# Performance work log

Hardware: AMD Instinct MI355X
Metric: run time of the kernel (lower is better)

The kernel has to match this reference:

```python
import jax, jax.numpy as jnp
import numpy as np
from jax import lax

DOWNSAMPLE = 4.0   # downsample_rate
THRESHOLD = 0.7    # score threshold
NMS_RANGE = 3      # maxpool NMS kernel


def setup_inputs() -> dict:
    key = jax.random.key(0)
    k1, k2 = jax.random.split(key)
    radiace_factor = jax.random.uniform(k1, (8, 80, 192, 192), dtype=jnp.float32)  # class heatmap
    box = jax.random.uniform(k2, (8, 4, 192, 192), dtype=jnp.float32)              # [dx, dy, w, h]
    return {"radiace_factor": radiace_factor, "box": box}


def _nms(heat, kernel):
    # max_pool2d(kernel, stride=1, padding=(kernel-1)//2) == SAME window max
    hmax = lax.reduce_window(heat, -jnp.inf, lax.max,
                             (1, 1, kernel, kernel), (1, 1, 1, 1), 'SAME')
    return heat * (hmax == heat).astype(heat.dtype)


def reference(radiace_factor, box):
    B, C, H, W = radiace_factor.shape
    r = jnp.float32(DOWNSAMPLE)

    heat = _nms(radiace_factor, NMS_RANGE)
    score = heat.max(axis=1)               # [B,H,W] max over categories
    mask = score > THRESHOLD               # [B,H,W] kept peaks

    # grid of (x=col, y=row) matching torch.where(inds)[::-1]
    gx, gy = jnp.meshgrid(jnp.arange(W, dtype=jnp.float32),
                          jnp.arange(H, dtype=jnp.float32), indexing='xy')
    grid = jnp.stack([gx, gy], axis=-1)    # [H,W,2]

    b = jnp.moveaxis(box, 1, -1)           # [B,H,W,4] = (dx,dy,w,h)
    center_xy = (grid + b[..., 0:2]) * r   # [B,H,W,2]
    wh = b[..., 2:4] * r

    lim = jnp.array([W * DOWNSAMPLE, H * DOWNSAMPLE], dtype=jnp.float32)
    x1y1 = jnp.clip(center_xy - wh * 0.5, 0.0, lim)
    x2y2 = jnp.clip(center_xy + wh * 0.5, 0.0, lim)
    boxes = jnp.concatenate([x1y1, x2y2 - x1y1], axis=-1)  # [B,H,W,4] (x1,y1,w,h)

    # Dense, jit-friendly equivalent of the per-batch gather: zero-out non-kept
    m = mask[..., None]
    boxes_kept = jnp.where(m, boxes, 0.0)
    scores_kept = jnp.where(mask, score, 0.0)
    center_kept = jnp.where(m, center_xy, 0.0)
    return boxes_kept, mask, scores_kept, center_kept
```

## Files before the change

kernel.cpp:

```cpp
#include <hip/hip_runtime.h>
#include <math.h>


#define BB 8
#define CC 80
#define HH 192
#define WW 192
#define SS 8
#define NBPIX (BB*HH*WW)

__global__ __launch_bounds__(256) void score_kernel(const float* __restrict__ heat,
                                                    float* __restrict__ part) {
    const int tid  = threadIdx.x;
    const int lane = tid & 63;
    const int wv   = tid >> 6;
    const int yt   = blockIdx.x;
    const int zs   = blockIdx.y;
    const int b    = blockIdx.z;
    const int y0   = yt * SS;
    const bool lok = lane < 48;
    const int  col0 = lane * 4;

    __shared__ float red[4][SS][WW];

    float4 sc[SS];
#pragma unroll
    for (int i = 0; i < SS; ++i) sc[i] = make_float4(0.f, 0.f, 0.f, 0.f);

    const int cbase = (zs * 4 + wv) * 10;
    const float NI = -INFINITY;

    for (int k = 0; k < 10; ++k) {
        const int c = cbase + k;
        const float* hp = heat + ((size_t)(b * CC + c) * HH) * WW;
        float4 v[SS + 2];
#pragma unroll
        for (int r = 0; r < SS + 2; ++r) {
            const int  row = y0 - 1 + r;
            const bool ok  = lok && ((unsigned)row < HH);
            v[r] = ok ? *reinterpret_cast<const float4*>(hp + row * WW + col0)
                      : make_float4(NI, NI, NI, NI);
        }
#pragma unroll
        for (int i = 0; i < SS; ++i) {
            const float4 a = v[i], m = v[i + 1], d = v[i + 2];
            float4 vm;
            vm.x = fmaxf(fmaxf(a.x, m.x), d.x);
            vm.y = fmaxf(fmaxf(a.y, m.y), d.y);
            vm.z = fmaxf(fmaxf(a.z, m.z), d.z);
            vm.w = fmaxf(fmaxf(a.w, m.w), d.w);

            float L = __shfl_up(vm.w, 1);
            float R = __shfl_down(vm.x, 1);
            if (lane == 0)  L = NI;
            if (lane >= 47) R = NI;

            float4 hm;
            hm.x = fmaxf(fmaxf(L,    vm.x), vm.y);
            hm.y = fmaxf(fmaxf(vm.x, vm.y), vm.z);
            hm.z = fmaxf(fmaxf(vm.y, vm.z), vm.w);
            hm.w = fmaxf(fmaxf(vm.z, vm.w), R);

            sc[i].x = fmaxf(sc[i].x, (m.x == hm.x) ? m.x : 0.0f);
            sc[i].y = fmaxf(sc[i].y, (m.y == hm.y) ? m.y : 0.0f);
            sc[i].z = fmaxf(sc[i].z, (m.z == hm.z) ? m.z : 0.0f);
            sc[i].w = fmaxf(sc[i].w, (m.w == hm.w) ? m.w : 0.0f);
        }
    }

    if (lok) {
#pragma unroll
        for (int i = 0; i < SS; ++i)
            *reinterpret_cast<float4*>(&red[wv][i][col0]) = sc[i];
    }
    __syncthreads();

    float* pp = part + ((size_t)(zs * BB + b) * HH + y0) * WW;
#pragma unroll
    for (int k = 0; k < SS * WW / 256; ++k) {
        const int idx = k * 256 + tid;
        const int row = idx / WW, col = idx - row * WW;
        const float mx = fmaxf(fmaxf(red[0][row][col], red[1][row][col]),
                               fmaxf(red[2][row][col], red[3][row][col]));
        pp[idx] = mx;
    }
}

__global__ __launch_bounds__(256) void decode_kernel(const float* __restrict__ box,
                                                     const float* __restrict__ part,
                                                     float* __restrict__ out) {
    const int pix = blockIdx.x * 256 + threadIdx.x;
    if (pix >= NBPIX) return;

    const int b   = pix / (HH * WW);
    const int rem = pix - b * (HH * WW);
    const int y   = rem / WW;
    const int x   = rem - y * WW;

    float* boxes  = out;
    float* maskp  = out + (size_t)4 * NBPIX;
    float* scorep = out + (size_t)5 * NBPIX;
    float* ctr    = out + (size_t)6 * NBPIX;

    const float s = fmaxf(part[pix], part[NBPIX + pix]);
    const bool  m = s > 0.7f;

    const float* bp = box + (size_t)b * 4 * HH * WW + rem;
    const float dx = bp[0];
    const float dy = bp[(size_t)HH * WW];
    const float bw = bp[(size_t)2 * HH * WW];
    const float bh = bp[(size_t)3 * HH * WW];

    const float cx = ((float)x + dx) * 4.0f;
    const float cy = ((float)y + dy) * 4.0f;
    const float w4 = bw * 4.0f;
    const float h4 = bh * 4.0f;
    const float lim = 768.0f;
    const float x1 = fminf(fmaxf(cx - w4 * 0.5f, 0.0f), lim);
    const float y1 = fminf(fmaxf(cy - h4 * 0.5f, 0.0f), lim);
    const float x2 = fminf(fmaxf(cx + w4 * 0.5f, 0.0f), lim);
    const float y2 = fminf(fmaxf(cy + h4 * 0.5f, 0.0f), lim);

    float4 bo;
    bo.x = m ? x1 : 0.0f;
    bo.y = m ? y1 : 0.0f;
    bo.z = m ? (x2 - x1) : 0.0f;
    bo.w = m ? (y2 - y1) : 0.0f;
    reinterpret_cast<float4*>(boxes)[pix] = bo;

    maskp[pix]  = m ? 1.0f : 0.0f;
    scorep[pix] = m ? s : 0.0f;

    float2 cc;
    cc.x = m ? cx : 0.0f;
    cc.y = m ? cy : 0.0f;
    reinterpret_cast<float2*>(ctr)[pix] = cc;
}

extern "C" void kernel_launch(void* const* d_in, const int* in_sizes, int n_in,
                              void* d_out, int out_size, void* d_ws, size_t ws_size,
                              hipStream_t stream) {
    const float* heat = (const float*)d_in[0];
    const float* box  = (const float*)d_in[1];
    float* out  = (float*)d_out;
    float* part = (float*)d_ws;

    dim3 g1(HH / SS, 2, BB);
    score_kernel<<<g1, 256, 0, stream>>>(heat, part);

    decode_kernel<<<NBPIX / 256, 256, 0, stream>>>(box, part, out);
}
```

Baseline: 147.8 us.

## Fuse score and decode kernels into one 512-thread kernel

Merges the NMS score reduction and the box decode into a single kernel. Each block now uses eight waves covering all 80 channels, so the channel-split partial buffer in workspace and its write/read round trip go away. Box inputs are prefetched before the barrier to overlap with the reduction. The row tile shrinks from 8 to 6 and the grid changes to 32x8 blocks of 512 threads, which gives fewer, larger blocks and could reduce occupancy or load balance on the device.

```diff
diff --git a/kernel.cpp b/kernel.cpp
--- a/kernel.cpp
+++ b/kernel.cpp
@@ -6,28 +6,29 @@
 #define CC 80
 #define HH 192
 #define WW 192
-#define SS 8
+#define SS 6
+#define NPIX (SS*WW)
 #define NBPIX (BB*HH*WW)
 
-__global__ __launch_bounds__(256) void score_kernel(const float* __restrict__ heat,
-                                                    float* __restrict__ part) {
+__global__ __launch_bounds__(512) void fused_kernel(const float* __restrict__ heat,
+                                                    const float* __restrict__ box,
+                                                    float* __restrict__ out) {
     const int tid  = threadIdx.x;
     const int lane = tid & 63;
     const int wv   = tid >> 6;
     const int yt   = blockIdx.x;
-    const int zs   = blockIdx.y;
-    const int b    = blockIdx.z;
+    const int b    = blockIdx.y;
     const int y0   = yt * SS;
     const bool lok = lane < 48;
     const int  col0 = lane * 4;
 
-    __shared__ float red[4][SS][WW];
+    __shared__ float red[8][SS][WW];
 
     float4 sc[SS];
 #pragma unroll
     for (int i = 0; i < SS; ++i) sc[i] = make_float4(0.f, 0.f, 0.f, 0.f);
 
-    const int cbase = (zs * 4 + wv) * 10;
+    const int cbase = wv * 10;
     const float NI = -INFINITY;
 
     for (int k = 0; k < 10; ++k) {
@@ -68,6 +69,20 @@
         }
     }
 
+    const int    pixbase = (b * HH + y0) * WW;
+    const float* bp0     = box + (size_t)b * 4 * HH * WW + (size_t)y0 * WW;
+    float pdx[3], pdy[3], pw[3], ph[3];
+#pragma unroll
+    for (int kk = 0; kk < 3; ++kk) {
+        const int idx = kk * 512 + tid;
+        if (idx < NPIX) {
+            pdx[kk] = bp0[idx];
+            pdy[kk] = bp0[idx + (size_t)HH * WW];
+            pw[kk]  = bp0[idx + (size_t)2 * HH * WW];
+            ph[kk]  = bp0[idx + (size_t)3 * HH * WW];
+        }
+    }
+
     if (lok) {
 #pragma unroll
         for (int i = 0; i < SS; ++i)
@@ -75,66 +90,54 @@
     }
     __syncthreads();
 
-    float* pp = part + ((size_t)(zs * BB + b) * HH + y0) * WW;
-#pragma unroll
-    for (int k = 0; k < SS * WW / 256; ++k) {
-        const int idx = k * 256 + tid;
-        const int row = idx / WW, col = idx - row * WW;
-        const float mx = fmaxf(fmaxf(red[0][row][col], red[1][row][col]),
-                               fmaxf(red[2][row][col], red[3][row][col]));
-        pp[idx] = mx;
-    }
-}
-
-__global__ __launch_bounds__(256) void decode_kernel(const float* __restrict__ box,
-                                                     const float* __restrict__ part,
-                                                     float* __restrict__ out) {
-    const int pix = blockIdx.x * 256 + threadIdx.x;
-    if (pix >= NBPIX) return;
-
-    const int b   = pix / (HH * WW);
-    const int rem = pix - b * (HH * WW);
-    const int y   = rem / WW;
-    const int x   = rem - y * WW;
-
     float* boxes  = out;
     float* maskp  = out + (size_t)4 * NBPIX;
     float* scorep = out + (size_t)5 * NBPIX;
     float* ctr    = out + (size_t)6 * NBPIX;
 
-    const float s = fmaxf(part[pix], part[NBPIX + pix]);
-    const bool  m = s > 0.7f;
+    const float* rf = &red[0][0][0];
 
-    const float* bp = box + (size_t)b * 4 * HH * WW + rem;
-    const float dx = bp[0];
-    const float dy = bp[(size_t)HH * WW];
-    const float bw = bp[(size_t)2 * HH * WW];
-    const float bh = bp[(size_t)3 * HH * WW];
+#pragma unroll
+    for (int kk = 0; kk < 3; ++kk) {
+        const int idx = kk * 512 + tid;
+        if (idx < NPIX) {
+            const int row = idx / WW;
+            const int x   = idx - row * WW;
+            const int y   = y0 + row;
 
-    const float cx = ((float)x + dx) * 4.0f;
-    const float cy = ((float)y + dy) * 4.0f;
-    const float w4 = bw * 4.0f;
-    const float h4 = bh * 4.0f;
-    const float lim = 768.0f;
-    const float x1 = fminf(fmaxf(cx - w4 * 0.5f, 0.0f), lim);
-    const float y1 = fminf(fmaxf(cy - h4 * 0.5f, 0.0f), lim);
-    const float x2 = fminf(fmaxf(cx + w4 * 0.5f, 0.0f), lim);
-    const float y2 = fminf(fmaxf(cy + h4 * 0.5f, 0.0f), lim);
+            float s = rf[idx];
+#pragma unroll
+            for (int w = 1; w < 8; ++w) s = fmaxf(s, rf[w * NPIX + idx]);
+            const bool m = s > 0.7f;
 
-    float4 bo;
-    bo.x = m ? x1 : 0.0f;
-    bo.y = m ? y1 : 0.0f;
-    bo.z = m ? (x2 - x1) : 0.0f;
-    bo.w = m ? (y2 - y1) : 0.0f;
-    reinterpret_cast<float4*>(boxes)[pix] = bo;
+            const float cx = ((float)x + pdx[kk]) * 4.0f;
+            const float cy = ((float)y + pdy[kk]) * 4.0f;
+            const float w4 = pw[kk] * 4.0f;
+            const float h4 = ph[kk] * 4.0f;
+            const float lim = 768.0f;
+            const float x1 = fminf(fmaxf(cx - w4 * 0.5f, 0.0f), lim);
+            const float y1 = fminf(fmaxf(cy - h4 * 0.5f, 0.0f), lim);
+            const float x2 = fminf(fmaxf(cx + w4 * 0.5f, 0.0f), lim);
+            const float y2 = fminf(fmaxf(cy + h4 * 0.5f, 0.0f), lim);
 
-    maskp[pix]  = m ? 1.0f : 0.0f;
-    scorep[pix] = m ? s : 0.0f;
+            const int pix = pixbase + idx;
 
-    float2 cc;
-    cc.x = m ? cx : 0.0f;
-    cc.y = m ? cy : 0.0f;
-    reinterpret_cast<float2*>(ctr)[pix] = cc;
+            float4 bo;
+            bo.x = m ? x1 : 0.0f;
+            bo.y = m ? y1 : 0.0f;
+            bo.z = m ? (x2 - x1) : 0.0f;
+            bo.w = m ? (y2 - y1) : 0.0f;
+            reinterpret_cast<float4*>(boxes)[pix] = bo;
+
+            maskp[pix]  = m ? 1.0f : 0.0f;
+            scorep[pix] = m ? s : 0.0f;
+
+            float2 cc;
+            cc.x = m ? cx : 0.0f;
+            cc.y = m ? cy : 0.0f;
+            reinterpret_cast<float2*>(ctr)[pix] = cc;
+        }
+    }
 }
 
 extern "C" void kernel_launch(void* const* d_in, const int* in_sizes, int n_in,
@@ -142,11 +145,8 @@
                               hipStream_t stream) {
     const float* heat = (const float*)d_in[0];
     const float* box  = (const float*)d_in[1];
-    float* out  = (float*)d_out;
-    float* part = (float*)d_ws;
+    float* out = (float*)d_out;
 
-    dim3 g1(HH / SS, 2, BB);
-    score_kernel<<<g1, 256, 0, stream>>>(heat, part);
-
-    decode_kernel<<<NBPIX / 256, 256, 0, stream>>>(box, part, out);
+    dim3 g(HH / SS, BB);
+    fused_kernel<<<g, 512, 0, stream>>>(heat, box, out);
 }
```

Result: no change. 145.6 us (-1.5%).
